# Optimization experiments

Hardware: AMD Instinct MI355X
Metric: run time of the kernel (lower is better)

Reference implementation:

```python
import jax, jax.numpy as jnp
import numpy as np

D_MODEL = 1024
N_HEADS = 16
D_HEAD = D_MODEL // N_HEADS


def setup_inputs() -> dict:
    key = jax.random.key(0)
    kx, kq, kk, kv = jax.random.split(key, 4)
    B, T = 2, 2048
    X = jax.random.normal(kx, (B, T, D_MODEL), dtype=jnp.float32)
    s = 1.0 / np.sqrt(D_MODEL)
    # torch nn.Linear weight is [out, in]; y = x @ W.T
    Wq = jax.random.uniform(kq, (D_MODEL, D_MODEL), jnp.float32, -s, s)
    Wk = jax.random.uniform(kk, (D_MODEL, D_MODEL), jnp.float32, -s, s)
    Wv = jax.random.uniform(kv, (D_MODEL, D_MODEL), jnp.float32, -s, s)
    return {"X": X, "Wq": Wq, "Wk": Wk, "Wv": Wv}


def reference(X, Wq, Wk, Wv):
    B, T, _ = X.shape
    def heads(W):
        # x @ W.T -> [B,T,D] -> [B,H,T,Dh]
        return (X @ W.T).reshape(B, T, N_HEADS, D_HEAD).transpose(0, 2, 1, 3)
    Q, K, V = heads(Wq), heads(Wk), heads(Wv)
    scores = jnp.einsum('bhqd,bhkd->bhqk', Q, K)
    causal = jnp.tril(jnp.ones((T, T), dtype=bool))
    # original masks with -inf BEFORE scaling; -inf/scale == -inf, so equivalent
    scores = jnp.where(causal, scores, -jnp.inf) / jnp.sqrt(jnp.float32(D_HEAD))
    attn = jax.nn.softmax(scores, axis=-1)
    out = jnp.einsum('bhqk,bhkd->bhqd', attn, V)
    return out.transpose(0, 2, 1, 3).reshape(B, T, N_HEADS * D_HEAD)
```

## Files before the change

kernel.cpp:

```cpp
#include <hip/hip_runtime.h>


using bf16x8  = __attribute__((ext_vector_type(8))) __bf16;
using floatx4 = __attribute__((ext_vector_type(4))) float;

#define T_SEQ   2048
#define D_MODEL 1024
#define N_HEADS 16
#define D_HEAD  64
#define BATCH   2
#define M_TOT   4096
#define N_TOT   3072
#define PLANE   (T_SEQ * D_HEAD)
#define NX      (M_TOT * D_MODEL)
#define NWSEG   (D_MODEL * D_MODEL)
#define QSCALE  0.18033688f
#define SM_BIAS 24.0f

__device__ __forceinline__ unsigned short f32_to_bf16(float f) {
  unsigned int u = __float_as_uint(f);
  u += 0x7fffu + ((u >> 16) & 1u);
  return (unsigned short)(u >> 16);
}
__device__ __forceinline__ unsigned int pack2_bf16(float a, float b) {
  unsigned int ua = __float_as_uint(a) + 0x8000u;
  unsigned int ub = __float_as_uint(b) + 0x8000u;
  return __builtin_amdgcn_perm(ub, ua, 0x07060302);
}
__device__ __forceinline__ void async_cp16(void* lds, const void* gptr) {
  __builtin_amdgcn_global_load_lds(
      (const __attribute__((address_space(1))) unsigned int*)gptr,
      (__attribute__((address_space(3))) unsigned int*)lds, 16, 0, 0);
}

__global__ __launch_bounds__(256) void cvt_kernel(
    const float* __restrict__ X,  const float* __restrict__ Wq,
    const float* __restrict__ Wk, const float* __restrict__ Wv,
    unsigned short* __restrict__ Xb, unsigned short* __restrict__ Wb)
{
  const size_t i = ((size_t)blockIdx.x * 256 + threadIdx.x) * 8;
  const float* src;
  unsigned short* dst;
  if (i < NX) { src = X + i; dst = Xb + i; }
  else {
    const size_t r = i - NX;
    const int w = (int)(r >> 20);
    const size_t o = r & (NWSEG - 1);
    src = ((w == 0) ? Wq : (w == 1) ? Wk : Wv) + o;
    dst = Wb + r;
  }
  float4 f0 = *(const float4*)src;
  float4 f1 = *(const float4*)(src + 4);
  uint4 out;
  out.x = pack2_bf16(f0.x, f0.y);
  out.y = pack2_bf16(f0.z, f0.w);
  out.z = pack2_bf16(f1.x, f1.y);
  out.w = pack2_bf16(f1.z, f1.w);
  *(uint4*)dst = out;
}

__global__ __launch_bounds__(256) void gemm_qkv(
    const unsigned short* __restrict__ Xb,
    const unsigned short* __restrict__ Wb,
    unsigned short* __restrict__ Qb,
    unsigned short* __restrict__ Kb,
    unsigned short* __restrict__ VTb)
{
  __shared__ unsigned short Als[128 * 64];
  __shared__ unsigned short Bls[128 * 64];

  const int tid  = threadIdx.x;
  const int lane = tid & 63;
  const int wave = tid >> 6;
  const int l15  = lane & 15;
  const int quad = lane >> 4;
  const int wm   = wave >> 1, wn = wave & 1;

  const int n_blk = blockIdx.x * 128;
  const int m_blk = blockIdx.y * 128;

  const int swz = (((tid >> 3) ^ tid) & 7) * 8;
  const unsigned short* Ag = Xb + (size_t)(m_blk + (tid >> 3)) * D_MODEL + swz;
  const unsigned short* Bg = Wb + (size_t)(n_blk + (tid >> 3)) * D_MODEL + swz;
  char* Alds = (char*)Als + wave * 1024;
  char* Blds = (char*)Bls + wave * 1024;

  floatx4 acc[4][4] = {};

  for (int k0 = 0; k0 < D_MODEL; k0 += 64) {
    __syncthreads();
#pragma unroll
    for (int p = 0; p < 4; p++) {
      async_cp16(Alds + p * 4096, Ag + (size_t)p * 32 * D_MODEL + k0);
      async_cp16(Blds + p * 4096, Bg + (size_t)p * 32 * D_MODEL + k0);
    }
    __syncthreads();

#pragma unroll
    for (int ks = 0; ks < 2; ks++) {
      bf16x8 a[4], b[4];
#pragma unroll
      for (int i = 0; i < 4; i++) {
        const int sa = ((ks * 4 + quad) ^ (l15 & 7)) * 16;
        a[i] = *(const bf16x8*)((char*)Als + (wm * 64 + 16 * i + l15) * 128 + sa);
        b[i] = *(const bf16x8*)((char*)Bls + (wn * 64 + 16 * i + l15) * 128 + sa);
      }
#pragma unroll
      for (int mi = 0; mi < 4; mi++)
#pragma unroll
        for (int ni = 0; ni < 4; ni++)
          acc[mi][ni] = __builtin_amdgcn_mfma_f32_16x16x32_bf16(a[mi], b[ni], acc[mi][ni], 0, 0, 0);
    }
  }

  __syncthreads();
  char* ep = (char*)Als + wave * 8192;
  const int w_sel  = n_blk >> 10;
  const int m_base = m_blk + wm * 64;
  const int n_base = n_blk + wn * 64;
  const int h      = (n_base & 1023) >> 6;
  const float csc  = (w_sel == 0) ? QSCALE : 1.0f;

  if (w_sel < 2) {
#pragma unroll
    for (int mi = 0; mi < 4; mi++)
#pragma unroll
      for (int ni = 0; ni < 4; ni++)
#pragma unroll
        for (int r = 0; r < 4; r++) {
          const int row  = 16 * mi + quad * 4 + r;
          const int colb = (16 * ni + l15) * 2;
          const int phys = ((colb >> 4) ^ (row & 7)) * 16;
          *(unsigned short*)(ep + row * 128 + phys + (colb & 15)) =
              f32_to_bf16(acc[mi][ni][r] * csc);
        }
  } else {
#pragma unroll
    for (int mi = 0; mi < 4; mi++)
#pragma unroll
      for (int ni = 0; ni < 4; ni++)
#pragma unroll
        for (int r = 0; r < 4; r++) {
          const int row  = 16 * ni + l15;
          const int colb = (16 * mi + quad * 4 + r) * 2;
          const int phys = ((colb >> 4) ^ (row & 7)) * 16;
          *(unsigned short*)(ep + row * 128 + phys + (colb & 15)) =
              f32_to_bf16(acc[mi][ni][r]);
        }
  }
  asm volatile("s_waitcnt lgkmcnt(0)" ::: "memory");

#pragma unroll
  for (int pass = 0; pass < 8; pass++) {
    const int row  = pass * 8 + (lane >> 3);
    const int phys = ((lane & 7) ^ (row & 7)) * 16;
    uint4 v = *(const uint4*)(ep + row * 128 + phys);
    if (w_sel < 2) {
      const int m  = m_base + row;
      const int bb = m >> 11;
      const int t  = m & (T_SEQ - 1);
      unsigned short* dst = ((w_sel == 0) ? Qb : Kb) +
          ((size_t)(bb * N_HEADS + h) * T_SEQ + t) * D_HEAD + (lane & 7) * 8;
      *(uint4*)dst = v;
    } else {
      const int bb = m_base >> 11;
      unsigned short* dst = VTb +
          ((size_t)(bb * N_HEADS + h) * D_HEAD + row) * T_SEQ + (m_base & (T_SEQ - 1)) + (lane & 7) * 8;
      *(uint4*)dst = v;
    }
  }
}

__global__ __launch_bounds__(256) void attn_kernel(
    const unsigned short* __restrict__ Qb,
    const unsigned short* __restrict__ Kb,
    const unsigned short* __restrict__ VTb,
    float* __restrict__ Out)
{
  __shared__ unsigned short Ks[2][64 * 64];
  __shared__ unsigned short Vs[2][64 * 64];
  __shared__ unsigned short Ps[4][16 * 64];

  const int tid  = threadIdx.x;
  const int lane = tid & 63;
  const int wave = tid >> 6;
  const int l15  = lane & 15;
  const int quad = lane >> 4;

  const int bh    = blockIdx.x & 31;
  const int strip = 31 - (blockIdx.x >> 5);
  const int q0w   = strip * 64 + wave * 16;
  const int nch   = strip + 1;

  const unsigned short* Qp = Qb  + (size_t)bh * PLANE;
  const unsigned short* Kp = Kb  + (size_t)bh * PLANE;
  const unsigned short* Vp = VTb + (size_t)bh * PLANE;

  const int swz = (((tid >> 3) ^ tid) & 7) * 8;
  const unsigned short* Kg = Kp + (size_t)(tid >> 3) * D_HEAD + swz;
  const unsigned short* Vg = Vp + (size_t)(tid >> 3) * T_SEQ + swz;
  unsigned short* myp = Ps[wave];
  const int b = bh >> 4, h = bh & 15;

  bf16x8 aq[2];
#pragma unroll
  for (int s = 0; s < 2; s++)
    aq[s] = *(const bf16x8*)(Qp + (size_t)(q0w + l15) * D_HEAD + 32 * s + quad * 8);

  float l_acc[4] = {};
  floatx4 o[4] = {};

#pragma unroll
  for (int p = 0; p < 2; p++) {
    async_cp16((char*)Ks[0] + p * 4096 + wave * 1024, Kg + (size_t)(p * 32) * D_HEAD);
    async_cp16((char*)Vs[0] + p * 4096 + wave * 1024, Vg + (size_t)(p * 32) * T_SEQ);
  }

  for (int jc = 0; jc < nch; jc++) {
    __syncthreads();
    if (jc + 1 < nch) {
      const int j1 = (jc + 1) * 64;
      char* kd = (char*)Ks[(jc + 1) & 1];
      char* vd = (char*)Vs[(jc + 1) & 1];
#pragma unroll
      for (int p = 0; p < 2; p++) {
        async_cp16(kd + p * 4096 + wave * 1024, Kg + (size_t)(j1 + p * 32) * D_HEAD);
        async_cp16(vd + p * 4096 + wave * 1024, Vg + (size_t)(p * 32) * T_SEQ + j1);
      }
    }
    const char* Ksb = (const char*)Ks[jc & 1];
    const char* Vsb = (const char*)Vs[jc & 1];

    floatx4 s[4] = {};
#pragma unroll
    for (int t = 0; t < 4; t++)
#pragma unroll
      for (int ss = 0; ss < 2; ss++) {
        const int sa = ((ss * 4 + quad) ^ (l15 & 7)) * 16;
        bf16x8 bk = *(const bf16x8*)(Ksb + (16 * t + l15) * 128 + sa);
        s[t] = __builtin_amdgcn_mfma_f32_16x16x32_bf16(aq[ss], bk, s[t], 0, 0, 0);
      }

    if (jc == nch - 1) {
      const int j0 = jc * 64;
#pragma unroll
      for (int t = 0; t < 4; t++) {
        const int kk = j0 + 16 * t + l15;
#pragma unroll
        for (int r = 0; r < 4; r++)
          if (kk > q0w + quad * 4 + r) s[t][r] = -INFINITY;
      }
    }

#pragma unroll
    for (int t = 0; t < 4; t++)
#pragma unroll
      for (int r = 0; r < 4; r++)
        s[t][r] = exp2f(s[t][r] - SM_BIAS);
#pragma unroll
    for (int r = 0; r < 4; r++)
      l_acc[r] += (s[0][r] + s[1][r]) + (s[2][r] + s[3][r]);

#pragma unroll
    for (int t = 0; t < 4; t++)
#pragma unroll
      for (int r = 0; r < 4; r++) {
        const int row  = quad * 4 + r;
        const int phys = ((2 * t + (l15 >> 3)) ^ (row & 7)) * 16;
        *(unsigned short*)((char*)myp + row * 128 + phys + (l15 & 7) * 2) =
            f32_to_bf16(s[t][r]);
      }
    asm volatile("s_waitcnt lgkmcnt(0)" ::: "memory");

#pragma unroll
    for (int ks = 0; ks < 2; ks++) {
      const int pa = ((ks * 4 + quad) ^ (l15 & 7)) * 16;
      bf16x8 ap = *(const bf16x8*)((char*)myp + l15 * 128 + pa);
#pragma unroll
      for (int n = 0; n < 4; n++) {
        const int sa = ((ks * 4 + quad) ^ (l15 & 7)) * 16;
        bf16x8 bv = *(const bf16x8*)(Vsb + (16 * n + l15) * 128 + sa);
        o[n] = __builtin_amdgcn_mfma_f32_16x16x32_bf16(ap, bv, o[n], 0, 0, 0);
      }
    }
  }

#pragma unroll
  for (int r = 0; r < 4; r++) {
#pragma unroll
    for (int d = 1; d < 16; d <<= 1) l_acc[r] += __shfl_xor(l_acc[r], d);
  }

#pragma unroll
  for (int r = 0; r < 4; r++) {
    const float inv_l = 1.0f / l_acc[r];
    const int t = q0w + quad * 4 + r;
#pragma unroll
    for (int n = 0; n < 4; n++)
      Out[(size_t)(b * T_SEQ + t) * D_MODEL + h * D_HEAD + 16 * n + l15] = o[n][r] * inv_l;
  }
}

extern "C" void kernel_launch(void* const* d_in, const int* in_sizes, int n_in,
                              void* d_out, int out_size, void* d_ws, size_t ws_size,
                              hipStream_t stream) {
  const float* X  = (const float*)d_in[0];
  const float* Wq = (const float*)d_in[1];
  const float* Wk = (const float*)d_in[2];
  const float* Wv = (const float*)d_in[3];

  unsigned short* Qb = (unsigned short*)d_ws;
  unsigned short* Kb = Qb + (size_t)BATCH * N_HEADS * T_SEQ * D_HEAD;
  unsigned short* VT = Kb + (size_t)BATCH * N_HEADS * T_SEQ * D_HEAD;

  unsigned short* Xb = (unsigned short*)d_out;
  unsigned short* Wb = Xb + (size_t)NX;

  cvt_kernel<<<3584, 256, 0, stream>>>(X, Wq, Wk, Wv, Xb, Wb);

  dim3 g1(N_TOT / 128, M_TOT / 128);
  gemm_qkv<<<g1, 256, 0, stream>>>(Xb, Wb, Qb, Kb, VT);

  attn_kernel<<<1024, 256, 0, stream>>>(Qb, Kb, VT, (float*)d_out);
}
```

Before: 161.5 us.

## Load K/V fragments directly from global into registers, per-wave query tiles

Attention waves now each own a 16-row query tile and load K and V MFMA operands straight from global memory into registers, dropping the shared-memory double buffer and block-wide barriers. Blocks shrink to two waves with twice as many blocks launched. This removes barrier and LDS staging costs and gives finer causal load balance, but K/V reuse across waves moves from LDS to cache and global load latency is no longer hidden by async prefetch.

```diff
diff --git a/kernel.cpp b/kernel.cpp
--- a/kernel.cpp
+++ b/kernel.cpp
@@ -171,15 +171,13 @@
   }
 }
 
-__global__ __launch_bounds__(256) void attn_kernel(
+__global__ __launch_bounds__(128) void attn_kernel(
     const unsigned short* __restrict__ Qb,
     const unsigned short* __restrict__ Kb,
     const unsigned short* __restrict__ VTb,
     float* __restrict__ Out)
 {
-  __shared__ unsigned short Ks[2][64 * 64];
-  __shared__ unsigned short Vs[2][64 * 64];
-  __shared__ unsigned short Ps[4][16 * 64];
+  __shared__ unsigned short Ps[2][16 * 64];
 
   const int tid  = threadIdx.x;
   const int lane = tid & 63;
@@ -187,68 +185,59 @@
   const int l15  = lane & 15;
   const int quad = lane >> 4;
 
-  const int bh    = blockIdx.x & 31;
-  const int strip = 31 - (blockIdx.x >> 5);
-  const int q0w   = strip * 64 + wave * 16;
-  const int nch   = strip + 1;
+  const int bh = blockIdx.x & 31;
+  const int qt = 126 - 2 * (blockIdx.x >> 5) + wave;
+  const int q0 = qt * 16;
+  const int nch = (qt >> 2) + 1;
 
   const unsigned short* Qp = Qb  + (size_t)bh * PLANE;
   const unsigned short* Kp = Kb  + (size_t)bh * PLANE;
   const unsigned short* Vp = VTb + (size_t)bh * PLANE;
-
-  const int swz = (((tid >> 3) ^ tid) & 7) * 8;
-  const unsigned short* Kg = Kp + (size_t)(tid >> 3) * D_HEAD + swz;
-  const unsigned short* Vg = Vp + (size_t)(tid >> 3) * T_SEQ + swz;
   unsigned short* myp = Ps[wave];
   const int b = bh >> 4, h = bh & 15;
 
   bf16x8 aq[2];
 #pragma unroll
   for (int s = 0; s < 2; s++)
-    aq[s] = *(const bf16x8*)(Qp + (size_t)(q0w + l15) * D_HEAD + 32 * s + quad * 8);
+    aq[s] = *(const bf16x8*)(Qp + (size_t)(q0 + l15) * D_HEAD + 32 * s + quad * 8);
 
   float l_acc[4] = {};
   floatx4 o[4] = {};
 
-#pragma unroll
-  for (int p = 0; p < 2; p++) {
-    async_cp16((char*)Ks[0] + p * 4096 + wave * 1024, Kg + (size_t)(p * 32) * D_HEAD);
-    async_cp16((char*)Vs[0] + p * 4096 + wave * 1024, Vg + (size_t)(p * 32) * T_SEQ);
-  }
+  const unsigned short* Kg = Kp + (size_t)l15 * D_HEAD + quad * 8;
+  const unsigned short* Vg = Vp + (size_t)(l15)*T_SEQ + quad * 8;
 
   for (int jc = 0; jc < nch; jc++) {
-    __syncthreads();
-    if (jc + 1 < nch) {
-      const int j1 = (jc + 1) * 64;
-      char* kd = (char*)Ks[(jc + 1) & 1];
-      char* vd = (char*)Vs[(jc + 1) & 1];
-#pragma unroll
-      for (int p = 0; p < 2; p++) {
-        async_cp16(kd + p * 4096 + wave * 1024, Kg + (size_t)(j1 + p * 32) * D_HEAD);
-        async_cp16(vd + p * 4096 + wave * 1024, Vg + (size_t)(p * 32) * T_SEQ + j1);
-      }
-    }
-    const char* Ksb = (const char*)Ks[jc & 1];
-    const char* Vsb = (const char*)Vs[jc & 1];
+    const int j0 = jc * 64;
+
+    bf16x8 bk[8];
+#pragma unroll
+    for (int t = 0; t < 4; t++)
+#pragma unroll
+      for (int ss = 0; ss < 2; ss++)
+        bk[t * 2 + ss] = *(const bf16x8*)(Kg + (size_t)(j0 + 16 * t) * D_HEAD + ss * 32);
 
     floatx4 s[4] = {};
 #pragma unroll
     for (int t = 0; t < 4; t++)
 #pragma unroll
-      for (int ss = 0; ss < 2; ss++) {
-        const int sa = ((ss * 4 + quad) ^ (l15 & 7)) * 16;
-        bf16x8 bk = *(const bf16x8*)(Ksb + (16 * t + l15) * 128 + sa);
-        s[t] = __builtin_amdgcn_mfma_f32_16x16x32_bf16(aq[ss], bk, s[t], 0, 0, 0);
-      }
+      for (int ss = 0; ss < 2; ss++)
+        s[t] = __builtin_amdgcn_mfma_f32_16x16x32_bf16(aq[ss], bk[t * 2 + ss], s[t], 0, 0, 0);
+
+    bf16x8 bv[8];
+#pragma unroll
+    for (int n = 0; n < 4; n++)
+#pragma unroll
+      for (int ks = 0; ks < 2; ks++)
+        bv[n * 2 + ks] = *(const bf16x8*)(Vg + (size_t)(16 * n) * T_SEQ + j0 + ks * 32);
 
     if (jc == nch - 1) {
-      const int j0 = jc * 64;
 #pragma unroll
       for (int t = 0; t < 4; t++) {
         const int kk = j0 + 16 * t + l15;
 #pragma unroll
         for (int r = 0; r < 4; r++)
-          if (kk > q0w + quad * 4 + r) s[t][r] = -INFINITY;
+          if (kk > q0 + quad * 4 + r) s[t][r] = -INFINITY;
       }
     }
 
@@ -277,11 +266,8 @@
       const int pa = ((ks * 4 + quad) ^ (l15 & 7)) * 16;
       bf16x8 ap = *(const bf16x8*)((char*)myp + l15 * 128 + pa);
 #pragma unroll
-      for (int n = 0; n < 4; n++) {
-        const int sa = ((ks * 4 + quad) ^ (l15 & 7)) * 16;
-        bf16x8 bv = *(const bf16x8*)(Vsb + (16 * n + l15) * 128 + sa);
-        o[n] = __builtin_amdgcn_mfma_f32_16x16x32_bf16(ap, bv, o[n], 0, 0, 0);
-      }
+      for (int n = 0; n < 4; n++)
+        o[n] = __builtin_amdgcn_mfma_f32_16x16x32_bf16(ap, bv[n * 2 + ks], o[n], 0, 0, 0);
     }
   }
 
@@ -294,7 +280,7 @@
 #pragma unroll
   for (int r = 0; r < 4; r++) {
     const float inv_l = 1.0f / l_acc[r];
-    const int t = q0w + quad * 4 + r;
+    const int t = q0 + quad * 4 + r;
 #pragma unroll
     for (int n = 0; n < 4; n++)
       Out[(size_t)(b * T_SEQ + t) * D_MODEL + h * D_HEAD + 16 * n + l15] = o[n][r] * inv_l;
@@ -321,5 +307,5 @@
   dim3 g1(N_TOT / 128, M_TOT / 128);
   gemm_qkv<<<g1, 256, 0, stream>>>(Xb, Wb, Qb, Kb, VT);
 
-  attn_kernel<<<1024, 256, 0, stream>>>(Qb, Kb, VT, (float*)d_out);
-}
+  attn_kernel<<<2048, 128, 0, stream>>>(Qb, Kb, VT, (float*)d_out);
+}
```

Result: slower. 240.9 us (+49.1%).
